# Performance work log

Measured on AMD Instinct MI355X. Metric: run time of the kernel, lower is better.

The kernel has to match this reference:

```python
import jax, jax.numpy as jnp
import numpy as np

B, T, C = 2, 2048, 1024
H = 16
HD = C // H  # head_dim = 64
SCALE = HD ** -0.5

def setup_inputs() -> dict:
    key = jax.random.key(0)
    ks = jax.random.split(key, 5)
    s = 1.0 / np.sqrt(C)
    return {
        "x": jax.random.normal(ks[0], (B, T, C), dtype=jnp.float32),
        "Wq": jax.random.normal(ks[1], (C, C), dtype=jnp.float32) * s,
        "Wk": jax.random.normal(ks[2], (C, C), dtype=jnp.float32) * s,
        "Wv": jax.random.normal(ks[3], (C, C), dtype=jnp.float32) * s,
        "Wp": jax.random.normal(ks[4], (C, C), dtype=jnp.float32) * s,
        "bp": jnp.zeros((C,), dtype=jnp.float32),
    }

def reference(x, Wq, Wk, Wv, Wp, bp):
    b, t, c = x.shape
    # QKV projections (no bias, qkv_bias=False) -> [B,T,H,HD]
    q = (x @ Wq).reshape(b, t, H, HD)
    k = (x @ Wk).reshape(b, t, H, HD)
    v = (x @ Wv).reshape(b, t, H, HD)
    # scores [B,H,T,T]
    scores = jnp.einsum("bqhd,bkhd->bhqk", q, k) * SCALE
    causal = jnp.tril(jnp.ones((t, t), dtype=bool))
    scores = jnp.where(causal, scores, -jnp.inf)
    attn = jax.nn.softmax(scores, axis=-1)  # dropout = identity (eval mode)
    out = jnp.einsum("bhqk,bkhd->bqhd", attn, v).reshape(b, t, c)
    return out @ Wp + bp
```

## Files before the change

### kernel.cpp

```cpp
#include <hip/hip_runtime.h>


typedef __attribute__((ext_vector_type(8))) short shortx8;
typedef __attribute__((ext_vector_type(4))) short shortx4;
typedef __attribute__((ext_vector_type(8))) unsigned short ushortx8;
typedef __attribute__((ext_vector_type(4))) float f32x4;
typedef __attribute__((ext_vector_type(16))) float f32x16;

#define MFMA16(a, b, c) __builtin_amdgcn_mfma_f32_16x16x32_bf16((a), (b), (c), 0, 0, 0)
#define MFMA32(a, b, c) __builtin_amdgcn_mfma_f32_32x32x16_bf16((a), (b), (c), 0, 0, 0)

#define SC_L2E 0.18033688011112042f

__device__ __forceinline__ unsigned short f2bf(float f) {
  union { float f; unsigned u; } v; v.f = f;
  unsigned r = v.u + 0x7fffu + ((v.u >> 16) & 1u);
  return (unsigned short)(r >> 16);
}

__device__ __forceinline__ float fexp2(float x) {
#if __has_builtin(__builtin_amdgcn_exp2f)
  return __builtin_amdgcn_exp2f(x);
#else
  return exp2f(x);
#endif
}

__device__ __forceinline__ void gload16(const void* g, void* l) {
  __builtin_amdgcn_global_load_lds(
      (const __attribute__((address_space(1))) void*)g,
      (__attribute__((address_space(3))) void*)l, 16, 0, 0);
}

__global__ __launch_bounds__(256) void cvt_x(const float* __restrict__ x,
                                             unsigned short* __restrict__ xb, int n4) {
  int i = blockIdx.x * 256 + threadIdx.x;
  if (i < n4) {
    float4 v = ((const float4*)x)[i];
    unsigned short* o = xb + (size_t)i * 4;
    o[0] = f2bf(v.x); o[1] = f2bf(v.y); o[2] = f2bf(v.z); o[3] = f2bf(v.w);
  }
}

__global__ __launch_bounds__(256) void transpose_w4(
    const float* __restrict__ Wq, const float* __restrict__ Wk,
    const float* __restrict__ Wv, const float* __restrict__ Wp,
    unsigned short* __restrict__ wqkvT, unsigned short* __restrict__ wpT) {
  __shared__ float tile[32][33];
  const int zi = blockIdx.z;
  const float* src = (zi == 0) ? Wq : (zi == 1) ? Wk : (zi == 2) ? Wv : Wp;
  unsigned short* dst = (zi == 3) ? wpT : wqkvT + (size_t)zi * 1048576;
  const int bx = blockIdx.x * 32, by = blockIdx.y * 32;
  const int tx = threadIdx.x & 31, ty = threadIdx.x >> 5;
  #pragma unroll
  for (int i = 0; i < 32; i += 8)
    tile[ty + i][tx] = src[(size_t)(by + ty + i) * 1024 + bx + tx];
  __syncthreads();
  #pragma unroll
  for (int i = 0; i < 32; i += 8)
    dst[(size_t)(bx + ty + i) * 1024 + by + tx] = f2bf(tile[tx][ty + i]);
}

__global__ __launch_bounds__(256) void gemm_bt(
    const unsigned short* __restrict__ A, const unsigned short* __restrict__ BT,
    unsigned short* __restrict__ Cb, float* __restrict__ Cf,
    const float* __restrict__ bias, int M, int N, int K,
    float qscale, int scale_cols, unsigned short* __restrict__ vTo) {
  __shared__ unsigned short As[128 * 32];
  __shared__ unsigned short Bs[128 * 32];
  const int tid = threadIdx.x;
  const int lane = tid & 63, w = tid >> 6;
  const int wr = w >> 1, wc = w & 1;
  const int brow = blockIdx.y << 7, bcol = blockIdx.x << 7;

  f32x4 z = {0.f, 0.f, 0.f, 0.f};
  f32x4 acc[4][4];
  #pragma unroll
  for (int m = 0; m < 4; ++m)
    #pragma unroll
    for (int n = 0; n < 4; ++n) acc[m][n] = z;

  const int srow = tid >> 2;
  const int scol = (tid & 3) << 3;
  const unsigned short* Ap = A + (size_t)(brow + srow) * K + scol;
  const unsigned short* Bp = BT + (size_t)(bcol + srow) * K + scol;
  unsigned short* AsW = &As[w * 512];
  unsigned short* BsW = &Bs[w * 512];
  const size_t rowK64 = (size_t)64 * K;

  for (int k0 = 0; k0 < K; k0 += 32) {
    gload16(Ap + k0, AsW);
    gload16(Ap + rowK64 + k0, AsW + 2048);
    gload16(Bp + k0, BsW);
    gload16(Bp + rowK64 + k0, BsW + 2048);
    __syncthreads();
    shortx8 af[4], bf[4];
    const int koff = (lane >> 4) << 3;
    const int ar = (wr << 6) + (lane & 15);
    const int br = (wc << 6) + (lane & 15);
    #pragma unroll
    for (int m = 0; m < 4; ++m) af[m] = *(const shortx8*)&As[(ar + m * 16) * 32 + koff];
    #pragma unroll
    for (int n = 0; n < 4; ++n) bf[n] = *(const shortx8*)&Bs[(br + n * 16) * 32 + koff];
    #pragma unroll
    for (int m = 0; m < 4; ++m)
      #pragma unroll
      for (int n = 0; n < 4; ++n) acc[m][n] = MFMA16(af[m], bf[n], acc[m][n]);
    __syncthreads();
  }

  const int r0 = (lane >> 4) << 2;
  const int c0 = lane & 15;
  if (Cb) {
    if (vTo && bcol >= 2048) {
      #pragma unroll
      for (int m = 0; m < 4; ++m)
        #pragma unroll
        for (int n = 0; n < 4; ++n) {
          const int dp = bcol - 2048 + (wc << 6) + n * 16 + c0;
          const size_t rowb = brow + (wr << 6) + m * 16 + r0;
          shortx4 o4;
          #pragma unroll
          for (int j = 0; j < 4; ++j) o4[j] = (short)f2bf(acc[m][n][j]);
          *(shortx4*)&vTo[(size_t)dp * 4096 + rowb] = o4;
        }
    } else {
      #pragma unroll
      for (int m = 0; m < 4; ++m)
        #pragma unroll
        for (int n = 0; n < 4; ++n)
          #pragma unroll
          for (int j = 0; j < 4; ++j) {
            const size_t row = brow + (wr << 6) + m * 16 + r0 + j;
            const size_t col = bcol + (wc << 6) + n * 16 + c0;
            float v = acc[m][n][j];
            if ((int)col < scale_cols) v *= qscale;
            Cb[row * N + col] = f2bf(v);
          }
    }
  } else {
    #pragma unroll
    for (int m = 0; m < 4; ++m)
      #pragma unroll
      for (int n = 0; n < 4; ++n)
        #pragma unroll
        for (int j = 0; j < 4; ++j) {
          const size_t row = brow + (wr << 6) + m * 16 + r0 + j;
          const size_t col = bcol + (wc << 6) + n * 16 + c0;
          Cf[row * N + col] = acc[m][n][j] + bias[col];
        }
  }
}


__global__ __launch_bounds__(128, 4) void attn_fwd(
    const unsigned short* __restrict__ qkv, const unsigned short* __restrict__ vT,
    unsigned short* __restrict__ att) {
  __shared__ unsigned short Ks[2][2][2048];
  __shared__ unsigned short Vt[2][2][2048];

  const int tid = threadIdx.x;
  const int lane = tid & 63;
  const int p = tid >> 6;
  const int stream = blockIdx.x;
  const int h = stream & 15, b = stream >> 4;
  const int qb = 63 - (int)blockIdx.y;
  const int ql = lane & 31;
  const int hi = lane >> 5;
  const int q = qb * 32 + ql;

  shortx8 qf[4];
  {
    const unsigned short* qp = qkv + ((size_t)(b * 2048 + q)) * 3072 + h * 64 + 8 * hi;
    #pragma unroll
    for (int kc = 0; kc < 4; ++kc) qf[kc] = *(const shortx8*)(qp + 16 * kc);
  }

  f32x16 z16;
  #pragma unroll
  for (int i = 0; i < 16; ++i) z16[i] = 0.f;
  f32x16 accO0 = z16, accO1 = z16;
  float m_run = -__builtin_inff(), l_run = 0.f;

  const unsigned short* kb[4];
  const unsigned short* vb[4];
  #pragma unroll
  for (int i = 0; i < 4; ++i) {
    const int krow = 8 * i + (lane >> 3);
    const int kcl = (lane & 7) ^ (((krow >> 1) ^ (krow >> 4)) & 7);
    kb[i] = qkv + ((size_t)(b * 2048 + krow)) * 3072 + 1024 + h * 64 + 8 * kcl;
    const int vrow = 16 * i + (lane >> 2);
    const int vcl = (lane & 3) ^ (((vrow >> 1) ^ (vrow >> 3)) & 3);
    vb[i] = vT + ((size_t)(h * 64 + vrow)) * 4096 + b * 2048 + 8 * vcl;
  }
  const int rs8 = ((ql >> 1) ^ (ql >> 4)) & 7;
  const int rs4 = ((ql >> 1) ^ (ql >> 3)) & 3;

  #define STAGE(t_, bi_)                                                    \
    do {                                                                    \
      _Pragma("unroll")                                                     \
      for (int i = 0; i < 4; ++i) {                                         \
        gload16(kb[i] + (size_t)(t_) * 32 * 3072, &Ks[p][bi_][i * 512]);    \
        gload16(vb[i] + (t_) * 32, &Vt[p][bi_][i * 512]);                   \
      }                                                                     \
    } while (0)

  int buf = 0;
  if (p <= qb) STAGE(p, 0);
  for (int t = p; t <= qb; t += 2) {
    if (t + 2 <= qb) {
      STAGE(t + 2, buf ^ 1);
      asm volatile("s_waitcnt vmcnt(8)" ::: "memory");
    } else {
      asm volatile("s_waitcnt vmcnt(0)" ::: "memory");
    }
    __builtin_amdgcn_sched_barrier(0);
    const unsigned short* K = &Ks[p][buf][0];
    const unsigned short* V = &Vt[p][buf][0];

    shortx8 kf[4];
    #pragma unroll
    for (int kc = 0; kc < 4; ++kc)
      kf[kc] = *(const shortx8*)&K[ql * 64 + 8 * ((2 * kc + hi) ^ rs8)];
    __builtin_amdgcn_s_setprio(1);
    f32x16 s = z16;
    #pragma unroll
    for (int kc = 0; kc < 4; ++kc) s = MFMA32(kf[kc], qf[kc], s);
    __builtin_amdgcn_s_setprio(0);

    shortx8 vf[2][2];
    #pragma unroll
    for (int dh = 0; dh < 2; ++dh)
      #pragma unroll
      for (int ks = 0; ks < 2; ++ks)
        vf[dh][ks] = *(const shortx8*)&V[(32 * dh + ql) * 32 + 8 * ((2 * ks + hi) ^ rs4)];

    if (t == qb) {
      #pragma unroll
      for (int r = 0; r < 16; ++r) {
        const int kvl = (r & 3) + 8 * (r >> 2) + 4 * hi;
        if (kvl > ql) s[r] = -__builtin_inff();
      }
    }

    float m8[8], m4[4];
    #pragma unroll
    for (int i = 0; i < 8; ++i) m8[i] = fmaxf(s[2 * i], s[2 * i + 1]);
    #pragma unroll
    for (int i = 0; i < 4; ++i) m4[i] = fmaxf(m8[2 * i], m8[2 * i + 1]);
    float mx = fmaxf(fmaxf(m4[0], m4[1]), fmaxf(m4[2], m4[3]));
    mx = fmaxf(mx, __shfl_xor(mx, 32));

    if (!__all(mx <= m_run + 8.0f)) {
      const float nm = fmaxf(m_run, mx);
      const float alpha = fexp2(m_run - nm);
      l_run *= alpha;
      #pragma unroll
      for (int r = 0; r < 16; ++r) { accO0[r] *= alpha; accO1[r] *= alpha; }
      m_run = nm;
    }

    #pragma unroll
    for (int r = 0; r < 16; ++r) s[r] = fexp2(s[r] - m_run);
    float a8[8], a4[4];
    #pragma unroll
    for (int i = 0; i < 8; ++i) a8[i] = s[2 * i] + s[2 * i + 1];
    #pragma unroll
    for (int i = 0; i < 4; ++i) a4[i] = a8[2 * i] + a8[2 * i + 1];
    float rsum = (a4[0] + a4[1]) + (a4[2] + a4[3]);
    rsum += __shfl_xor(rsum, 32);
    l_run += rsum;

    unsigned wv[8], xv[8];
    #pragma unroll
    for (int i = 0; i < 8; ++i)
      asm("v_cvt_pk_bf16_f32 %0, %1, %2" : "=v"(wv[i]) : "v"(s[2 * i]), "v"(s[2 * i + 1]));
    #pragma unroll
    for (int i = 0; i < 8; ++i) xv[i] = __shfl_xor(wv[i], 32);
    __builtin_amdgcn_s_setprio(1);
    #pragma unroll
    for (int ss = 0; ss < 2; ++ss) {
      union { unsigned u[4]; shortx8 s8; } pb;
      pb.u[0] = hi ? xv[4 * ss + 2] : wv[4 * ss];
      pb.u[1] = hi ? xv[4 * ss + 3] : wv[4 * ss + 1];
      pb.u[2] = hi ? wv[4 * ss + 2] : xv[4 * ss];
      pb.u[3] = hi ? wv[4 * ss + 3] : xv[4 * ss + 1];
      accO0 = MFMA32(vf[0][ss], pb.s8, accO0);
      accO1 = MFMA32(vf[1][ss], pb.s8, accO1);
    }
    __builtin_amdgcn_s_setprio(0);
    buf ^= 1;
  }
  #undef STAGE

  __syncthreads();
  float* mb = (float*)&Ks[0][0][0];
  float* ml = (float*)&Vt[0][0][0];
  if (p == 1) {
    #pragma unroll
    for (int rg = 0; rg < 4; ++rg) {
      f32x4 v0 = {accO0[4 * rg], accO0[4 * rg + 1], accO0[4 * rg + 2], accO0[4 * rg + 3]};
      f32x4 v1 = {accO1[4 * rg], accO1[4 * rg + 1], accO1[4 * rg + 2], accO1[4 * rg + 3]};
      *(f32x4*)&mb[(rg * 64 + lane) * 4] = v0;
      *(f32x4*)&mb[((4 + rg) * 64 + lane) * 4] = v1;
    }
    ml[lane] = m_run;
    ml[64 + lane] = l_run;
  }
  __syncthreads();
  if (p == 0) {
    const float m1 = ml[lane], l1 = ml[64 + lane];
    const float mf = fmaxf(m_run, m1);
    const float a0 = fexp2(m_run - mf);
    const float a1 = fexp2(m1 - mf);
    const float inv = 1.f / (l_run * a0 + l1 * a1);
    unsigned short* op = att + ((size_t)(b * 2048 + q)) * 1024 + h * 64;
    #pragma unroll
    for (int rq = 0; rq < 4; ++rq) {
      f32x4 p0 = *(const f32x4*)&mb[(rq * 64 + lane) * 4];
      f32x4 p1 = *(const f32x4*)&mb[((4 + rq) * 64 + lane) * 4];
      shortx4 o0, o1;
      #pragma unroll
      for (int j = 0; j < 4; ++j) {
        o0[j] = (short)f2bf((accO0[4 * rq + j] * a0 + p0[j] * a1) * inv);
        o1[j] = (short)f2bf((accO1[4 * rq + j] * a0 + p1[j] * a1) * inv);
      }
      *(shortx4*)&op[8 * rq + 4 * hi] = o0;
      *(shortx4*)&op[32 + 8 * rq + 4 * hi] = o1;
    }
  }
}

extern "C" void kernel_launch(void* const* d_in, const int* in_sizes, int n_in,
                              void* d_out, int out_size, void* d_ws, size_t ws_size,
                              hipStream_t stream) {
  const float* x  = (const float*)d_in[0];
  const float* Wq = (const float*)d_in[1];
  const float* Wk = (const float*)d_in[2];
  const float* Wv = (const float*)d_in[3];
  const float* Wp = (const float*)d_in[4];
  const float* bp = (const float*)d_in[5];

  char* ws = (char*)d_ws;
  unsigned short* xb    = (unsigned short*)(ws);
  unsigned short* wqkvT = (unsigned short*)(ws + (size_t)8  * 1048576);
  unsigned short* wpT   = (unsigned short*)(ws + (size_t)14 * 1048576);
  unsigned short* qkv   = (unsigned short*)(ws + (size_t)16 * 1048576);
  unsigned short* vT    = (unsigned short*)(ws + (size_t)40 * 1048576);
  unsigned short* att   = (unsigned short*)(ws + (size_t)48 * 1048576);

  cvt_x<<<dim3(4096), dim3(256), 0, stream>>>(x, xb, 1048576);
  transpose_w4<<<dim3(32, 32, 4), dim3(256), 0, stream>>>(Wq, Wk, Wv, Wp, wqkvT, wpT);
  gemm_bt<<<dim3(24, 32), dim3(256), 0, stream>>>(xb, wqkvT, qkv, nullptr, nullptr,
                                                  4096, 3072, 1024, SC_L2E, 1024, vT);
  attn_fwd<<<dim3(32, 64), dim3(128), 0, stream>>>(qkv, vT, att);
  gemm_bt<<<dim3(8, 32), dim3(256), 0, stream>>>(att, wpT, nullptr, (float*)d_out, bp,
                                                 4096, 1024, 1024, 0.f, 0, nullptr);
}
```

Before: 129.9 us.

## Single-buffer K/V tiles in attention to halve shared memory footprint

```diff
diff --git a/kernel.cpp b/kernel.cpp
--- a/kernel.cpp
+++ b/kernel.cpp
@@ -156,8 +156,7 @@
 __global__ __launch_bounds__(128, 4) void attn_fwd(
     const unsigned short* __restrict__ qkv, const unsigned short* __restrict__ vT,
     unsigned short* __restrict__ att) {
-  __shared__ unsigned short Ks[2][2][2048];
-  __shared__ unsigned short Vt[2][2][2048];
+  __shared__ unsigned short sh[2][4096];
 
   const int tid = threadIdx.x;
   const int lane = tid & 63;
@@ -196,44 +195,43 @@
   const int rs8 = ((ql >> 1) ^ (ql >> 4)) & 7;
   const int rs4 = ((ql >> 1) ^ (ql >> 3)) & 3;
 
-  #define STAGE(t_, bi_)                                                    \
-    do {                                                                    \
-      _Pragma("unroll")                                                     \
-      for (int i = 0; i < 4; ++i) {                                         \
-        gload16(kb[i] + (size_t)(t_) * 32 * 3072, &Ks[p][bi_][i * 512]);    \
-        gload16(vb[i] + (t_) * 32, &Vt[p][bi_][i * 512]);                   \
-      }                                                                     \
+  unsigned short* Kl = &sh[p][0];
+  unsigned short* Vl = &sh[p][2048];
+
+  #define STAGE(t_)                                                        \
+    do {                                                                   \
+      _Pragma("unroll")                                                    \
+      for (int i = 0; i < 4; ++i) {                                        \
+        gload16(kb[i] + (size_t)(t_) * 32 * 3072, Kl + i * 512);           \
+        gload16(vb[i] + (t_) * 32, Vl + i * 512);                          \
+      }                                                                    \
     } while (0)
 
-  int buf = 0;
-  if (p <= qb) STAGE(p, 0);
+  if (p <= qb) STAGE(p);
   for (int t = p; t <= qb; t += 2) {
-    if (t + 2 <= qb) {
-      STAGE(t + 2, buf ^ 1);
-      asm volatile("s_waitcnt vmcnt(8)" ::: "memory");
-    } else {
-      asm volatile("s_waitcnt vmcnt(0)" ::: "memory");
-    }
+    asm volatile("s_waitcnt vmcnt(0)" ::: "memory");
     __builtin_amdgcn_sched_barrier(0);
-    const unsigned short* K = &Ks[p][buf][0];
-    const unsigned short* V = &Vt[p][buf][0];
 
     shortx8 kf[4];
     #pragma unroll
     for (int kc = 0; kc < 4; ++kc)
-      kf[kc] = *(const shortx8*)&K[ql * 64 + 8 * ((2 * kc + hi) ^ rs8)];
+      kf[kc] = *(const shortx8*)&Kl[ql * 64 + 8 * ((2 * kc + hi) ^ rs8)];
+    shortx8 vf[2][2];
+    #pragma unroll
+    for (int dh = 0; dh < 2; ++dh)
+      #pragma unroll
+      for (int ks = 0; ks < 2; ++ks)
+        vf[dh][ks] = *(const shortx8*)&Vl[(32 * dh + ql) * 32 + 8 * ((2 * ks + hi) ^ rs4)];
+    asm volatile("s_waitcnt lgkmcnt(0)" ::: "memory");
+    __builtin_amdgcn_sched_barrier(0);
+
+    if (t + 2 <= qb) STAGE(t + 2);
+
     __builtin_amdgcn_s_setprio(1);
     f32x16 s = z16;
     #pragma unroll
     for (int kc = 0; kc < 4; ++kc) s = MFMA32(kf[kc], qf[kc], s);
     __builtin_amdgcn_s_setprio(0);
-
-    shortx8 vf[2][2];
-    #pragma unroll
-    for (int dh = 0; dh < 2; ++dh)
-      #pragma unroll
-      for (int ks = 0; ks < 2; ++ks)
-        vf[dh][ks] = *(const shortx8*)&V[(32 * dh + ql) * 32 + 8 * ((2 * ks + hi) ^ rs4)];
 
     if (t == qb) {
       #pragma unroll
@@ -289,13 +287,12 @@
       accO1 = MFMA32(vf[1][ss], pb.s8, accO1);
     }
     __builtin_amdgcn_s_setprio(0);
-    buf ^= 1;
   }
   #undef STAGE
 
   __syncthreads();
-  float* mb = (float*)&Ks[0][0][0];
-  float* ml = (float*)&Vt[0][0][0];
+  float* mb = (float*)&sh[0][0];
+  float* ml = mb + 2048;
   if (p == 1) {
     #pragma unroll
     for (int rg = 0; rg < 4; ++rg) {
```

Measured after the change: 124.8 us. -3.9%, faster.
